# Performance work log

Measured on AMD Instinct MI355X. Metric: run time of the kernel, lower is better.

Reference implementation:

```python
import jax, jax.numpy as jnp
import numpy as np

H = 8    # heads
DH = 64  # dim_head


def _attn(q, k, v):
    sim = jnp.einsum('bid,bjd->bij', q, k)
    a = jax.nn.softmax(sim, axis=-1)
    return jnp.einsum('bij,bjd->bid', a, v)


def setup_inputs() -> dict:
    key = jax.random.key(0)
    k1, k2, k3 = jax.random.split(key, 3)
    B, f, n, dim = 8, 16, 196, 512
    N = 1 + f * n  # cls token + f*n patch tokens
    x = jax.random.normal(k1, (B, N, dim), jnp.float32)
    W_qkv = jax.random.normal(k2, (dim, 3 * H * DH), jnp.float32) * 0.02
    W_out = jax.random.normal(k3, (H * DH, dim), jnp.float32) * 0.02
    b_out = jnp.zeros((dim,), jnp.float32)
    return {"x": x, "W_qkv": W_qkv, "W_out": W_out, "b_out": b_out, "f": f, "n": n}


def reference(x, W_qkv, W_out, b_out, f, n):
    B, N, dim = x.shape
    scale = DH ** -0.5
    qkv = x @ W_qkv                                   # [B, N, 3*H*DH]
    q, k, v = jnp.split(qkv, 3, axis=-1)
    # 'b n (h d) -> (b h) n d'
    to_bh = lambda t: t.reshape(B, N, H, DH).transpose(0, 2, 1, 3).reshape(B * H, N, DH)
    q, k, v = map(to_bh, (q, k, v))
    q = q * scale
    cls_q, q_ = q[:, :1], q[:, 1:]
    cls_k, k_ = k[:, :1], k[:, 1:]
    cls_v, v_ = v[:, :1], v[:, 1:]
    # cls token attends to everything
    cls_out = _attn(cls_q, k, v)                      # [B*H, 1, DH]
    # 'b (f n) d -> (b n) f d'
    to_time = lambda t: t.reshape(B * H, f, n, DH).transpose(0, 2, 1, 3).reshape(B * H * n, f, DH)
    q_, k_, v_ = map(to_time, (q_, k_, v_))
    # repeat cls k/v to each spatial location: 'b () d -> (b r) () d', r = n
    rep = lambda t: jnp.broadcast_to(t[:, None], (B * H, n, 1, DH)).reshape(B * H * n, 1, DH)
    k_ = jnp.concatenate([rep(cls_k), k_], axis=1)    # [B*H*n, f+1, DH]
    v_ = jnp.concatenate([rep(cls_v), v_], axis=1)
    out = _attn(q_, k_, v_)                           # [B*H*n, f, DH]
    # '(b n) f d -> b (f n) d'
    out = out.reshape(B * H, n, f, DH).transpose(0, 2, 1, 3).reshape(B * H, f * n, DH)
    out = jnp.concatenate([cls_out, out], axis=1)     # [B*H, N, DH]
    # '(b h) n d -> b n (h d)'
    out = out.reshape(B, H, N, DH).transpose(0, 2, 1, 3).reshape(B, N, H * DH)
    return out @ W_out + b_out
```

## Files before the change

kernel.cpp:

```cpp
#include <hip/hip_runtime.h>
#include <hip/hip_bf16.h>

#define B_    8
#define H_    8
#define DH_   64
#define FR    16
#define SP    196
#define NTOK  3137
#define DIM   512
#define NQKV  1536
#define MREAL (B_ * NTOK)
#define MPAD  25216

#define CSPLIT 50
#define CTOK   64

typedef __bf16 bf16x8 __attribute__((ext_vector_type(8)));
typedef float  f32x4  __attribute__((ext_vector_type(4)));
typedef unsigned short ushort8 __attribute__((ext_vector_type(8)));

__device__ __forceinline__ float bf2f(unsigned short u) {
    union { unsigned int i; float f; } x; x.i = ((unsigned int)u) << 16; return x.f;
}
__device__ __forceinline__ unsigned short f2bf(float f) {
    __hip_bfloat16 h = __float2bfloat16(f);
    union { __hip_bfloat16 h; unsigned short u; } x; x.h = h; return x.u;
}


__global__ __launch_bounds__(256) void convert_pad_x(const float* __restrict__ x,
                                                     unsigned short* __restrict__ xb) {
    int idx = blockIdx.x * 256 + threadIdx.x;
    const int real8 = MREAL * DIM / 8;
    ushort8 o;
    if (idx < real8) {
        f32x4 a = *(const f32x4*)(x + (size_t)idx * 8);
        f32x4 b = *(const f32x4*)(x + (size_t)idx * 8 + 4);
        o[0] = f2bf(a[0]); o[1] = f2bf(a[1]); o[2] = f2bf(a[2]); o[3] = f2bf(a[3]);
        o[4] = f2bf(b[0]); o[5] = f2bf(b[1]); o[6] = f2bf(b[2]); o[7] = f2bf(b[3]);
    } else {
        o = (ushort8){0,0,0,0,0,0,0,0};
    }
    *(ushort8*)(xb + (size_t)idx * 8) = o;
}

__global__ __launch_bounds__(256) void transpose_w(const float* __restrict__ W,
                                                   unsigned short* __restrict__ WT,
                                                   int K, int Nn) {
    __shared__ float tile[32][33];
    int n0 = blockIdx.x * 32, k0 = blockIdx.y * 32;
    int tx = threadIdx.x & 31, ty = threadIdx.x >> 5;
#pragma unroll
    for (int r = 0; r < 32; r += 8)
        tile[ty + r][tx] = W[(size_t)(k0 + ty + r) * Nn + n0 + tx];
    __syncthreads();
#pragma unroll
    for (int r = 0; r < 32; r += 8)
        WT[(size_t)(n0 + ty + r) * K + k0 + tx] = f2bf(tile[tx][ty + r]);
}

__global__ __launch_bounds__(256) void zero_pad_attn(unsigned short* __restrict__ attn) {
    int idx = blockIdx.x * 256 + threadIdx.x;
    ushort8 z = (ushort8){0,0,0,0,0,0,0,0};
    *(ushort8*)(attn + (size_t)MREAL * DIM + (size_t)idx * 8) = z;
}


__device__ __forceinline__ void gload_lds16(const unsigned short* g, unsigned short* l) {
    __builtin_amdgcn_global_load_lds((const __attribute__((address_space(1))) void*)g,
                                     (__attribute__((address_space(3))) void*)l, 16, 0, 0);
}

template<int EPI>
__global__ __launch_bounds__(256)
void gemm_bt(const unsigned short* __restrict__ A, const unsigned short* __restrict__ Bt,
             unsigned short* __restrict__ Cb, float* __restrict__ Cf,
             const float* __restrict__ bias, int Nn, int K) {
    __shared__ __attribute__((aligned(16))) unsigned short As[128 * 32];
    __shared__ __attribute__((aligned(16))) unsigned short Bs[128 * 32];
    int wave = threadIdx.x >> 6, lane = threadIdx.x & 63;
    int wm = wave >> 1, wn = wave & 1;
    int tM = blockIdx.x, tN = blockIdx.y;
    const int r15 = lane & 15, kq = (lane >> 4) * 8;
    f32x4 acc[4][4] = {};

    for (int k0 = 0; k0 < K; k0 += 32) {
#pragma unroll
        for (int r = 0; r < 2; ++r) {
            int chunk = (r * 4 + wave) * 64;
            int ce = chunk + lane;
            int row = ce >> 2, kp = (ce & 3) * 8;
            gload_lds16(A  + (size_t)(tM * 128 + row) * K + k0 + kp, As + chunk * 8);
            gload_lds16(Bt + (size_t)(tN * 128 + row) * K + k0 + kp, Bs + chunk * 8);
        }
        __syncthreads();
        bf16x8 af[4], bg[4];
#pragma unroll
        for (int m = 0; m < 4; m++)
            af[m] = *(const bf16x8*)&As[(wm * 64 + m * 16 + r15) * 32 + kq];
#pragma unroll
        for (int nn = 0; nn < 4; nn++)
            bg[nn] = *(const bf16x8*)&Bs[(wn * 64 + nn * 16 + r15) * 32 + kq];
#pragma unroll
        for (int m = 0; m < 4; m++)
#pragma unroll
            for (int nn = 0; nn < 4; nn++)
                acc[m][nn] = __builtin_amdgcn_mfma_f32_16x16x32_bf16(af[m], bg[nn], acc[m][nn], 0, 0, 0);
        __syncthreads();
    }

    int rowBase = tM * 128 + wm * 64 + (lane >> 4) * 4;
    int colBase = tN * 128 + wn * 64 + r15;
#pragma unroll
    for (int m = 0; m < 4; m++) {
#pragma unroll
        for (int nn = 0; nn < 4; nn++) {
            int col = colBase + nn * 16;
#pragma unroll
            for (int i = 0; i < 4; i++) {
                int row = rowBase + m * 16 + i;
                float v = acc[m][nn][i];
                if constexpr (EPI == 0) {
                    if (col < DIM) v *= 0.125f;
                    Cb[(size_t)row * Nn + col] = f2bf(v);
                } else {
                    if (row < MREAL) Cf[(size_t)row * Nn + col] = v + bias[col];
                }
            }
        }
    }
}

__global__ __launch_bounds__(256) void cls_partial(const unsigned short* __restrict__ qkv,
                                                   float* __restrict__ part) {
    int bh = blockIdx.y, split = blockIdx.x;
    int b = bh >> 3, h = bh & 7;
    int tid = threadIdx.x;
    size_t base = (size_t)b * NTOK * NQKV + h * 64;
    int t0 = split * CTOK;

    __shared__ float qls[64];
    __shared__ float sim[CTOK];
    __shared__ __attribute__((aligned(16))) unsigned short Vs[CTOK][64];
    __shared__ float red[256];
    __shared__ float Ms, Ss;

    if (tid < 64) qls[tid] = bf2f(qkv[base + tid]);

    {
        int t = tid >> 2, q = tid & 3;
        size_t g = base + (size_t)(t0 + t) * NQKV + 1024 + q * 16;
        *(ushort8*)&Vs[t][q * 16]     = *(const ushort8*)(qkv + g);
        *(ushort8*)&Vs[t][q * 16 + 8] = *(const ushort8*)(qkv + g + 8);
    }
    __syncthreads();

    float pacc = 0.f;
    {
        int t = tid >> 2, q = tid & 3;
        size_t g = base + (size_t)(t0 + t) * NQKV + 512 + q * 16;
        bf16x8 k0 = *(const bf16x8*)(qkv + g);
        bf16x8 k1 = *(const bf16x8*)(qkv + g + 8);
#pragma unroll
        for (int e = 0; e < 8; e++) {
            pacc += qls[q * 16 + e]     * (float)k0[e];
            pacc += qls[q * 16 + 8 + e] * (float)k1[e];
        }
    }
    pacc += __shfl_xor(pacc, 1);
    pacc += __shfl_xor(pacc, 2);
    if ((tid & 3) == 0) {
        int t = tid >> 2;
        sim[t] = (t0 + t < NTOK) ? pacc : -1e30f;
    }
    __syncthreads();

    if (tid < 64) {
        float m = sim[tid];
#pragma unroll
        for (int off = 32; off > 0; off >>= 1) m = fmaxf(m, __shfl_xor(m, off));
        float p = __expf(sim[tid] - m);
        sim[tid] = p;
        float s = p;
#pragma unroll
        for (int off = 32; off > 0; off >>= 1) s += __shfl_xor(s, off);
        if (tid == 0) { Ms = m; Ss = s; }
    }
    __syncthreads();

    int d = tid & 63, grp = tid >> 6;
    float acc = 0.f;
#pragma unroll
    for (int t = grp * 16; t < grp * 16 + 16; t++)
        acc += sim[t] * bf2f(Vs[t][d]);
    red[tid] = acc; __syncthreads();
    if (tid < 64) {
        float pv = red[tid] + red[tid + 64] + red[tid + 128] + red[tid + 192];
        float* pp = part + ((size_t)bh * CSPLIT + split) * 66;
        pp[2 + tid] = pv;
        if (tid == 0) { pp[0] = Ms; pp[1] = Ss; }
    }
}

__global__ __launch_bounds__(64) void cls_reduce(const float* __restrict__ part,
                                                 unsigned short* __restrict__ attn) {
    int bh = blockIdx.x, b = bh >> 3, h = bh & 7;
    int d = threadIdx.x;
    const float* pp = part + (size_t)bh * CSPLIT * 66;
    float M = -1e30f;
    for (int i = 0; i < CSPLIT; i++) M = fmaxf(M, pp[i * 66]);
    float S = 0.f, PV = 0.f;
    for (int i = 0; i < CSPLIT; i++) {
        float w = __expf(pp[i * 66] - M);
        S  += pp[i * 66 + 1] * w;
        PV += pp[i * 66 + 2 + d] * w;
    }
    attn[(size_t)(b * NTOK) * DIM + h * 64 + d] = f2bf(PV / S);
}

__global__ __launch_bounds__(256) void time_attn(const unsigned short* __restrict__ qkv,
                                                 unsigned short* __restrict__ attn) {
    int wave = threadIdx.x >> 6, lane = threadIdx.x & 63;
    int seq = blockIdx.x * 4 + wave;
    int bh = seq / SP, s = seq % SP;
    int b = bh >> 3, h = bh & 7;
    __shared__ __attribute__((aligned(16))) unsigned short Q[4][16][72];
    __shared__ __attribute__((aligned(16))) unsigned short Kt[4][17][72];
    __shared__ __attribute__((aligned(16))) unsigned short Vt[4][17][72];
    __shared__ float S[4][16][18];
    size_t base = (size_t)b * NTOK * NQKV + h * 64;

#pragma unroll
    for (int c = lane; c < 128; c += 64) {
        int i = c >> 3, part = c & 7;
        size_t g = base + (size_t)(1 + i * SP + s) * NQKV + part * 8;
        *(ushort8*)&Q[wave][i][part * 8] = *(const ushort8*)(qkv + g);
    }
    for (int c = lane; c < 136; c += 64) {
        int j = c >> 3, part = c & 7;
        int t = (j == 0) ? 0 : (1 + (j - 1) * SP + s);
        size_t g = base + (size_t)t * NQKV + part * 8;
        *(ushort8*)&Kt[wave][j][part * 8] = *(const ushort8*)(qkv + g + 512);
        *(ushort8*)&Vt[wave][j][part * 8] = *(const ushort8*)(qkv + g + 1024);
    }
    __syncthreads();

    for (int p = lane; p < 272; p += 64) {
        int i = p / 17, j = p - i * 17;
        float acc = 0.f;
#pragma unroll
        for (int c = 0; c < 8; c++) {
            bf16x8 qv = *(const bf16x8*)&Q[wave][i][c * 8];
            bf16x8 kv = *(const bf16x8*)&Kt[wave][j][c * 8];
#pragma unroll
            for (int e = 0; e < 8; e++) acc += (float)qv[e] * (float)kv[e];
        }
        S[wave][i][j] = acc;
    }
    __syncthreads();

    if (lane < 16) {
        int i = lane;
        float m = -1e30f;
#pragma unroll
        for (int j = 0; j < 17; j++) m = fmaxf(m, S[wave][i][j]);
        float sum = 0.f;
#pragma unroll
        for (int j = 0; j < 17; j++) {
            float p = __expf(S[wave][i][j] - m);
            S[wave][i][j] = p; sum += p;
        }
        float invs = 1.f / sum;
#pragma unroll
        for (int j = 0; j < 17; j++) S[wave][i][j] *= invs;
    }
    __syncthreads();

#pragma unroll
    for (int i = 0; i < 16; i++) {
        float acc = 0.f;
#pragma unroll
        for (int j = 0; j < 17; j++)
            acc += S[wave][i][j] * bf2f(Vt[wave][j][lane]);
        attn[(size_t)(b * NTOK + 1 + i * SP + s) * DIM + h * 64 + lane] = f2bf(acc);
    }
}


extern "C" void kernel_launch(void* const* d_in, const int* in_sizes, int n_in,
                              void* d_out, int out_size, void* d_ws, size_t ws_size,
                              hipStream_t stream) {
    (void)in_sizes; (void)n_in; (void)out_size; (void)ws_size;
    const float* x    = (const float*)d_in[0];
    const float* Wqkv = (const float*)d_in[1];
    const float* Wout = (const float*)d_in[2];
    const float* bout = (const float*)d_in[3];
    float* out = (float*)d_out;

    unsigned short* xb    = (unsigned short*)d_ws;
    unsigned short* qkv   = xb    + (size_t)MPAD * DIM;
    unsigned short* attn  = qkv   + (size_t)MPAD * NQKV;
    unsigned short* wqkvT = attn  + (size_t)MPAD * DIM;
    unsigned short* woutT = wqkvT + (size_t)NQKV * DIM;
    float* clspart = (float*)xb;

    convert_pad_x<<<MPAD * DIM / 8 / 256, 256, 0, stream>>>(x, xb);
    transpose_w<<<dim3(NQKV / 32, DIM / 32), 256, 0, stream>>>(Wqkv, wqkvT, DIM, NQKV);
    transpose_w<<<dim3(DIM / 32, DIM / 32), 256, 0, stream>>>(Wout, woutT, DIM, DIM);
    zero_pad_attn<<<(MPAD - MREAL) * DIM / 8 / 256, 256, 0, stream>>>(attn);

    gemm_bt<0><<<dim3(MPAD / 128, NQKV / 128), 256, 0, stream>>>(
        xb, wqkvT, qkv, nullptr, nullptr, NQKV, DIM);

    cls_partial<<<dim3(CSPLIT, B_ * H_), 256, 0, stream>>>(qkv, clspart);
    cls_reduce<<<B_ * H_, 64, 0, stream>>>(clspart, attn);
    time_attn<<<(B_ * H_ * SP) / 4, 256, 0, stream>>>(qkv, attn);

    gemm_bt<1><<<dim3(MPAD / 128, DIM / 128), 256, 0, stream>>>(
        attn, woutT, nullptr, out, bout, DIM, DIM);
}
```

Measured before the change: 315.2 us.

## Double-buffer GEMM LDS tiles and swizzle block order for L2 reuse

```diff
diff --git a/kernel.cpp b/kernel.cpp
--- a/kernel.cpp
+++ b/kernel.cpp
@@ -71,55 +71,86 @@
                                      (__attribute__((address_space(3))) void*)l, 16, 0, 0);
 }
 
+#define PATCH_M 16
+
 template<int EPI>
 __global__ __launch_bounds__(256)
 void gemm_bt(const unsigned short* __restrict__ A, const unsigned short* __restrict__ Bt,
              unsigned short* __restrict__ Cb, float* __restrict__ Cf,
-             const float* __restrict__ bias, int Nn, int K) {
-    __shared__ __attribute__((aligned(16))) unsigned short As[128 * 32];
-    __shared__ __attribute__((aligned(16))) unsigned short Bs[128 * 32];
+             const float* __restrict__ bias, int Nn, int K, int nM, int nN) {
+    __shared__ __attribute__((aligned(16))) unsigned short As[2][128 * 32];
+    __shared__ __attribute__((aligned(16))) unsigned short Bs[2][128 * 32];
+
+    int id = blockIdx.x;
+    int pid = id / (PATCH_M * nN);
+    int rem = id - pid * (PATCH_M * nN);
+    int m0 = pid * PATCH_M;
+    int pm = min(PATCH_M, nM - m0);
+    int tM = m0 + (rem % pm);
+    int tN = rem / pm;
+
     int wave = threadIdx.x >> 6, lane = threadIdx.x & 63;
     int wm = wave >> 1, wn = wave & 1;
-    int tM = blockIdx.x, tN = blockIdx.y;
     const int r15 = lane & 15, kq = (lane >> 4) * 8;
     f32x4 acc[4][4] = {};
 
-    for (int k0 = 0; k0 < K; k0 += 32) {
-#pragma unroll
-        for (int r = 0; r < 2; ++r) {
-            int chunk = (r * 4 + wave) * 64;
-            int ce = chunk + lane;
-            int row = ce >> 2, kp = (ce & 3) * 8;
-            gload_lds16(A  + (size_t)(tM * 128 + row) * K + k0 + kp, As + chunk * 8);
-            gload_lds16(Bt + (size_t)(tN * 128 + row) * K + k0 + kp, Bs + chunk * 8);
-        }
-        __syncthreads();
+    const unsigned short* Abase = A  + (size_t)(tM * 128) * K;
+    const unsigned short* Bbase = Bt + (size_t)(tN * 128) * K;
+
+    const int ce0 = wave * 64 + lane;
+    const int ce1 = ce0 + 256;
+
+#define STAGE(buf, k0)                                                          \
+    {                                                                           \
+        _Pragma("unroll")                                                       \
+        for (int r = 0; r < 2; ++r) {                                           \
+            int chunk = (r * 4 + wave) * 64;                                    \
+            int ce = chunk + lane;                                              \
+            int row = ce >> 2, kp = (ce & 3) * 8;                               \
+            gload_lds16(Abase + (size_t)row * K + (k0) + kp, &As[buf][chunk * 8]); \
+            gload_lds16(Bbase + (size_t)row * K + (k0) + kp, &Bs[buf][chunk * 8]); \
+        }                                                                       \
+    }
+
+    STAGE(0, 0)
+    asm volatile("s_waitcnt vmcnt(0)" ::: "memory");
+    __builtin_amdgcn_s_barrier();
+
+    const int nK = K / 32;
+    int cur = 0;
+    for (int kt = 0; kt < nK; ++kt) {
+        if (kt + 1 < nK) STAGE(cur ^ 1, (kt + 1) * 32)
         bf16x8 af[4], bg[4];
 #pragma unroll
         for (int m = 0; m < 4; m++)
-            af[m] = *(const bf16x8*)&As[(wm * 64 + m * 16 + r15) * 32 + kq];
-#pragma unroll
-        for (int nn = 0; nn < 4; nn++)
-            bg[nn] = *(const bf16x8*)&Bs[(wn * 64 + nn * 16 + r15) * 32 + kq];
+            af[m] = *(const bf16x8*)&As[cur][(wm * 64 + m * 16 + r15) * 32 + kq];
+#pragma unroll
+        for (int nn2 = 0; nn2 < 4; nn2++)
+            bg[nn2] = *(const bf16x8*)&Bs[cur][(wn * 64 + nn2 * 16 + r15) * 32 + kq];
+        __builtin_amdgcn_s_setprio(1);
 #pragma unroll
         for (int m = 0; m < 4; m++)
 #pragma unroll
-            for (int nn = 0; nn < 4; nn++)
-                acc[m][nn] = __builtin_amdgcn_mfma_f32_16x16x32_bf16(af[m], bg[nn], acc[m][nn], 0, 0, 0);
-        __syncthreads();
-    }
+            for (int nn2 = 0; nn2 < 4; nn2++)
+                acc[m][nn2] = __builtin_amdgcn_mfma_f32_16x16x32_bf16(af[m], bg[nn2], acc[m][nn2], 0, 0, 0);
+        __builtin_amdgcn_s_setprio(0);
+        asm volatile("s_waitcnt vmcnt(0)" ::: "memory");
+        __builtin_amdgcn_s_barrier();
+        cur ^= 1;
+    }
+#undef STAGE
 
     int rowBase = tM * 128 + wm * 64 + (lane >> 4) * 4;
     int colBase = tN * 128 + wn * 64 + r15;
 #pragma unroll
     for (int m = 0; m < 4; m++) {
 #pragma unroll
-        for (int nn = 0; nn < 4; nn++) {
-            int col = colBase + nn * 16;
+        for (int nn2 = 0; nn2 < 4; nn2++) {
+            int col = colBase + nn2 * 16;
 #pragma unroll
             for (int i = 0; i < 4; i++) {
                 int row = rowBase + m * 16 + i;
-                float v = acc[m][nn][i];
+                float v = acc[m][nn2][i];
                 if constexpr (EPI == 0) {
                     if (col < DIM) v *= 0.125f;
                     Cb[(size_t)row * Nn + col] = f2bf(v);
@@ -309,13 +340,14 @@
     transpose_w<<<dim3(DIM / 32, DIM / 32), 256, 0, stream>>>(Wout, woutT, DIM, DIM);
     zero_pad_attn<<<(MPAD - MREAL) * DIM / 8 / 256, 256, 0, stream>>>(attn);
 
-    gemm_bt<0><<<dim3(MPAD / 128, NQKV / 128), 256, 0, stream>>>(
-        xb, wqkvT, qkv, nullptr, nullptr, NQKV, DIM);
+    const int nM = MPAD / 128;
+    gemm_bt<0><<<nM * (NQKV / 128), 256, 0, stream>>>(
+        xb, wqkvT, qkv, nullptr, nullptr, NQKV, DIM, nM, NQKV / 128);
 
     cls_partial<<<dim3(CSPLIT, B_ * H_), 256, 0, stream>>>(qkv, clspart);
     cls_reduce<<<B_ * H_, 64, 0, stream>>>(clspart, attn);
     time_attn<<<(B_ * H_ * SP) / 4, 256, 0, stream>>>(qkv, attn);
 
-    gemm_bt<1><<<dim3(MPAD / 128, DIM / 128), 256, 0, stream>>>(
-        attn, woutT, nullptr, out, bout, DIM, DIM);
-}
+    gemm_bt<1><<<nM * (DIM / 128), 256, 0, stream>>>(
+        attn, woutT, nullptr, out, bout, DIM, DIM, nM, DIM / 128);
+}
```

Measured after the change: 298.6 us. 1.06x faster.
